# Performance work log

Hardware: AMD Instinct MI355X
Metric: run time of the kernel (lower is better)

Reference implementation:

```python
import jax, jax.numpy as jnp
from jax import lax
import numpy as np

B, N, H, T, NPB = 1024, 50, 128, 50, 3
C_TANH, NEG = 10.0, 1e9


def _lstm(x, h, c, Wi, Wh, b):
    gates = x @ Wi + h @ Wh + b
    i, f, g, o = jnp.split(gates, 4, axis=-1)
    c2 = jax.nn.sigmoid(f) * c + jax.nn.sigmoid(i) * jnp.tanh(g)
    return jax.nn.sigmoid(o) * jnp.tanh(c2), c2


def setup_inputs() -> dict:
    key = jax.random.key(0)
    ks = jax.random.split(key, 20)
    rn = lambda k, shape, fan: (jax.random.normal(k, shape, jnp.float32) / np.float32(np.sqrt(fan)))
    return {
        'input_pnt': jax.random.uniform(ks[0], (B, N, 2), jnp.float32),
        'W_emb': rn(ks[1], (2, H), 2), 'b_emb': jnp.zeros((H,), jnp.float32),
        'dec_init': rn(ks[2], (1, 1, H), H),
        'Wi': rn(ks[3], (H, 4 * H), H), 'Wh': rn(ks[4], (H, 4 * H), H), 'b_lstm': jnp.zeros((4 * H,), jnp.float32),
        'Wq_g': rn(ks[5], (H, H), H), 'Wref_g': rn(ks[6], (H, H), H), 'v_g': rn(ks[7], (H,), H),
        'Wq_p': rn(ks[8], (H, H), H), 'Wref_p': rn(ks[9], (H, H), H), 'v_p': rn(ks[10], (H,), H),
        'Wi_c': rn(ks[11], (H, 4 * H), H), 'Wh_c': rn(ks[12], (H, 4 * H), H), 'b_c': jnp.zeros((4 * H,), jnp.float32),
        'Wq_c': rn(ks[13], (H, H), H), 'Wref_c': rn(ks[14], (H, H), H), 'v_c': rn(ks[15], (H,), H),
        'W1': rn(ks[16], (H, H), H), 'b1': jnp.zeros((H,), jnp.float32),
        'W2': rn(ks[17], (H, 1), H), 'b2': jnp.zeros((1,), jnp.float32),
    }


def _forward(input_pnt, W_emb, b_emb, dec_init, Wi, Wh, b_lstm, Wq_g, Wref_g, v_g,
             Wq_p, Wref_p, v_p, Wi_c, Wh_c, b_c, Wq_c, Wref_c, v_c, W1, b1, W2, b2):
    context = input_pnt @ W_emb + b_emb                    # [B,N,H] embedded nodes
    e_g = context @ Wref_g                                  # glimpse keys (step-invariant, hoisted)
    e_p = context @ Wref_p                                  # pointer keys (hoisted)
    z = jnp.zeros((B, H), context.dtype)
    carry0 = (z, z, jnp.zeros((B, N), context.dtype), jnp.broadcast_to(dec_init[0, 0], (B, H)))

    def step(carry, _):
        h, c, mask, dec_in = carry
        h2, c2 = _lstm(dec_in, h, c, Wi, Wh, b_lstm)
        # glimpse attention (masked)
        q = h2 @ Wq_g
        u = jnp.einsum('bnh,h->bn', jnp.tanh(e_g + q[:, None, :]), v_g) - NEG * mask
        g = jnp.einsum('bn,bnh->bh', jax.nn.softmax(u, -1), e_g)
        # pointer attention with tanh exploration clipping (masked)
        u2 = jnp.einsum('bnh,h->bn', jnp.tanh(e_p + (g @ Wq_p)[:, None, :]), v_p)
        logit = C_TANH * jnp.tanh(u2) - NEG * mask
        logprob = jax.nn.log_softmax(logit, -1)
        prob = jax.nn.softmax(logit, -1)
        action = jnp.argmax(prob, -1)                       # greedy decode
        mask2 = jnp.maximum(mask, jax.nn.one_hot(action, N, dtype=mask.dtype))
        dec_next = jnp.take_along_axis(context, action[:, None, None], axis=1)[:, 0]
        coords = jnp.take_along_axis(input_pnt, action[:, None, None], axis=1)[:, 0]
        return (h2, c2, mask2, dec_next), (logprob, prob, action, coords)

    (_, _, _, dec_last), (logprobs, probs, actions, coords) = lax.scan(step, carry0, None, length=T)
    logprobs = jnp.transpose(logprobs, (1, 0, 2))           # [B,T,N]
    probs = jnp.transpose(probs, (1, 0, 2))
    actions = jnp.transpose(actions, (1, 0))                # [B,T]
    coords = jnp.transpose(coords, (1, 0, 2))               # [B,T,2] visited coordinates
    # reward: TSP tour length
    seg = coords[:, 1:] - coords[:, :-1]
    close = coords[:, 0] - coords[:, -1]
    R = jnp.sum(jnp.sqrt(jnp.sum(seg * seg, -1) + 1e-10), -1) + jnp.sqrt(jnp.sum(close * close, -1) + 1e-10)
    # critic: one LSTM step on last action broadcast to hidden, cn[0], then process blocks
    a4c = jnp.broadcast_to(actions[:, -1].astype(context.dtype)[:, None], (B, H))
    _, hy = _lstm(a4c, z, z, Wi_c, Wh_c, b_c)
    enc = dec_last[:, None, :]                              # context gathered at last action, [B,1,H]
    e_c = enc @ Wref_c
    for _ in range(NPB):
        u = jnp.einsum('bnh,h->bn', jnp.tanh(e_c + (hy @ Wq_c)[:, None, :]), v_c)
        hy = jnp.einsum('bn,bnh->bh', jax.nn.softmax(C_TANH * jnp.tanh(u), -1), e_c)
    v = (jax.nn.relu(hy @ W1 + b1) @ W2 + b2)[:, 0]
    return R, v, logprobs, actions, coords, probs


def reference(input_pnt, W_emb, b_emb, dec_init, Wi, Wh, b_lstm, Wq_g, Wref_g, v_g,
              Wq_p, Wref_p, v_p, Wi_c, Wh_c, b_c, Wq_c, Wref_c, v_c, W1, b1, W2, b2):
    return _forward(input_pnt, W_emb, b_emb, dec_init, Wi, Wh, b_lstm, Wq_g, Wref_g, v_g,
                    Wq_p, Wref_p, v_p, Wi_c, Wh_c, b_c, Wq_c, Wref_c, v_c, W1, b1, W2, b2)
```

## Files before the change

### kernel.cpp

```cpp
#include <hip/hip_runtime.h>
#include <math.h>

#define Bsz 1024
#define Npt 50
#define Hd 128
#define G4 512
#define Tt 50
#define NEGC 1000000000.0f
#define CTANH 10.0f

#define OFF_R 0
#define OFF_V 1024
#define OFF_LP 2048
#define OFF_A 2562048
#define OFF_C 2613248
#define OFF_P 2715648

#define WS_TG 0
#define WS_TP 512
#define WS_TQ 1024
#define WS_A0 1536
#define WS_A1 2048
#define WS_A2 2560
#define WS_A3 3072
#define WS_CT 3584

__device__ __forceinline__ float fsig(float x) {
  return __builtin_amdgcn_rcpf(1.0f + __expf(-x));
}

__device__ __forceinline__ float ftanh(float x) {
  float e = __expf(2.0f * x);
  return 1.0f - 2.0f * __builtin_amdgcn_rcpf(e + 1.0f);
}

__device__ __forceinline__ float dpp_sum_bcast(float x) {
  int v;
  v = __builtin_amdgcn_update_dpp(0, __float_as_int(x), 0x111, 0xf, 0xf, true);
  x += __int_as_float(v);
  v = __builtin_amdgcn_update_dpp(0, __float_as_int(x), 0x112, 0xf, 0xf, true);
  x += __int_as_float(v);
  v = __builtin_amdgcn_update_dpp(0, __float_as_int(x), 0x114, 0xf, 0xf, true);
  x += __int_as_float(v);
  v = __builtin_amdgcn_update_dpp(0, __float_as_int(x), 0x118, 0xf, 0xf, true);
  x += __int_as_float(v);
  v = __builtin_amdgcn_update_dpp(0, __float_as_int(x), 0x142, 0xf, 0xf, true);
  x += __int_as_float(v);
  v = __builtin_amdgcn_update_dpp(0, __float_as_int(x), 0x143, 0xf, 0xf, true);
  x += __int_as_float(v);
  return __int_as_float(__builtin_amdgcn_readlane(__float_as_int(x), 63));
}

__device__ __forceinline__ float dpp_max_bcast(float x) {
  int v;
  v = __builtin_amdgcn_update_dpp(0, __float_as_int(x), 0x111, 0xf, 0xf, true);
  x = fmaxf(x, __int_as_float(v));
  v = __builtin_amdgcn_update_dpp(0, __float_as_int(x), 0x112, 0xf, 0xf, true);
  x = fmaxf(x, __int_as_float(v));
  v = __builtin_amdgcn_update_dpp(0, __float_as_int(x), 0x114, 0xf, 0xf, true);
  x = fmaxf(x, __int_as_float(v));
  v = __builtin_amdgcn_update_dpp(0, __float_as_int(x), 0x118, 0xf, 0xf, true);
  x = fmaxf(x, __int_as_float(v));
  v = __builtin_amdgcn_update_dpp(0, __float_as_int(x), 0x142, 0xf, 0xf, true);
  x = fmaxf(x, __int_as_float(v));
  v = __builtin_amdgcn_update_dpp(0, __float_as_int(x), 0x143, 0xf, 0xf, true);
  x = fmaxf(x, __int_as_float(v));
  return __int_as_float(__builtin_amdgcn_readlane(__float_as_int(x), 63));
}

__device__ __forceinline__ float xsum(float x) {
  #pragma unroll
  for (int off = 32; off >= 1; off >>= 1) x += __shfl_xor(x, off, 64);
  return x;
}

__global__ __launch_bounds__(512) void k_pre(const float* __restrict__ Wemb,
                                             const float* __restrict__ bemb,
                                             const float* __restrict__ dinit,
                                             const float* __restrict__ Wi,
                                             const float* __restrict__ bl,
                                             const float* __restrict__ Wqp,
                                             const float* __restrict__ Wrg,
                                             const float* __restrict__ Wrp,
                                             const float* __restrict__ vg,
                                             const float* __restrict__ vp,
                                             const float* __restrict__ Wrc,
                                             const float* __restrict__ W1,
                                             const float* __restrict__ b1,
                                             const float* __restrict__ W2,
                                             float* __restrict__ ws) {
  __shared__ float mg_s[2][128], mp_s[2][128], cg_s[128], cp_s[128];
  __shared__ float pg_s[2][128], pc_s[128];
  __shared__ float r0_s[128], r1_s[128], rc_s[128];
  int t = threadIdx.x;
  if (t < 256) {
    int j = t >> 7, hh = t & 127;
    float ag = 0.f, ap = 0.f;
    for (int k = 0; k < 128; ++k) {
      float we = Wemb[j * 128 + k];
      ag = fmaf(we, Wrg[k * 128 + hh], ag);
      ap = fmaf(we, Wrp[k * 128 + hh], ap);
    }
    mg_s[j][hh] = ag; mp_s[j][hh] = ap;
  } else if (t < 384) {
    int hh = t & 127;
    float cgv = 0.f, cpv = 0.f;
    for (int k = 0; k < 128; ++k) {
      float be = bemb[k];
      cgv = fmaf(be, Wrg[k * 128 + hh], cgv);
      cpv = fmaf(be, Wrp[k * 128 + hh], cpv);
    }
    cg_s[hh] = cgv; cp_s[hh] = cpv;
  } else {
    int hh = t & 127;
    float a0 = 0.f, a1 = 0.f, ac = 0.f;
    for (int k = 0; k < 128; ++k) {
      float wr = Wrc[k * 128 + hh];
      a0 = fmaf(Wemb[k], wr, a0);
      a1 = fmaf(Wemb[128 + k], wr, a1);
      ac = fmaf(bemb[k], wr, ac);
    }
    r0_s[hh] = a0; r1_s[hh] = a1; rc_s[hh] = ac;
  }
  __syncthreads();
  if (t < 256) {
    int j = t >> 7, hh = t & 127;
    float pg = 0.f;
    for (int k = 0; k < 128; ++k) pg = fmaf(mg_s[j][k], Wqp[k * 128 + hh], pg);
    pg_s[j][hh] = pg;
  } else if (t < 384) {
    int hh = t & 127;
    float pcv = 0.f;
    for (int k = 0; k < 128; ++k) pcv = fmaf(cg_s[k], Wqp[k * 128 + hh], pcv);
    pc_s[hh] = pcv + cp_s[hh];
  } else {
    int hh = t & 127;
    float t0 = 0.f, t1 = 0.f, tc = 0.f;
    for (int k = 0; k < 128; ++k) {
      float w1 = W1[k * 128 + hh];
      t0 = fmaf(r0_s[k], w1, t0);
      t1 = fmaf(r1_s[k], w1, t1);
      tc = fmaf(rc_s[k], w1, tc);
    }
    float4* w4 = (float4*)ws;
    w4[WS_CT / 4 + hh] = make_float4(t0, t1, tc + b1[hh], W2[hh]);
  }
  __syncthreads();
  if (t < 128) {
    float4* w4 = (float4*)ws;
    w4[WS_TG / 4 + t] = make_float4(mg_s[0][t], mg_s[1][t], vg[t], cg_s[t]);
    w4[WS_TP / 4 + t] = make_float4(mp_s[0][t], mp_s[1][t], vp[t], cp_s[t]);
    w4[WS_TQ / 4 + t] = make_float4(pg_s[0][t], pg_s[1][t], pc_s[t], 0.f);
  }
  {
    int j = t;
    float a0 = 0.f, a1 = 0.f, a2 = 0.f, a3 = 0.f;
    for (int k = 0; k < 128; ++k) {
      float wi = Wi[k * G4 + j];
      a0 = fmaf(Wemb[k], wi, a0);
      a1 = fmaf(Wemb[128 + k], wi, a1);
      a2 = fmaf(bemb[k], wi, a2);
      a3 = fmaf(dinit[k], wi, a3);
    }
    ws[WS_A0 + j] = a0;
    ws[WS_A1 + j] = a1;
    ws[WS_A2 + j] = a2 + bl[j];
    ws[WS_A3 + j] = a3 + bl[j];
  }
}

__global__ __launch_bounds__(1024, 4) void k_mega(const float* __restrict__ ip,
                                                  const float* __restrict__ Wh,
                                                  const float* __restrict__ Wqg,
                                                  const float* __restrict__ b2,
                                                  const float* __restrict__ ws,
                                                  float* __restrict__ out) {
  __shared__ __align__(16) float gpart[8][4][G4];
  __shared__ __align__(16) float qpart[8][4][Hd];
  __shared__ __align__(16) float up_s[16][4][64];
  __shared__ __align__(16) float q_w[16][32];
  __shared__ __align__(16) float qp_s[Hd * 4];
  __shared__ __align__(16) float h_s[4][Hd];
  __shared__ __align__(16) float c_s[4][Hd];
  __shared__ __align__(16) float tg_s[G4];
  __shared__ __align__(16) float tp_s[G4];
  __shared__ __align__(16) float tq_s[G4];
  __shared__ __align__(16) float ct_s[G4];
  __shared__ __align__(16) float a0_s[G4], a1_s[G4], a2_s[G4], a3_s[G4];
  __shared__ __align__(16) float cg_s[Hd];
  __shared__ __align__(16) float ip_s[4][Npt * 2];
  __shared__ float mask_s[4][Npt];
  __shared__ float ch_s[4][Npt * 2];
  __shared__ float sel_s[4][2];

  int t = threadIdx.x, blk = blockIdx.x;
  int w = t >> 6, lane = t & 63;
  int kh = t >> 7, jt = t & 127;

  float4 wv[16];
  #pragma unroll
  for (int j = 0; j < 16; ++j)
    wv[j] = *(const float4*)&Wh[(kh * 16 + j) * G4 + jt * 4];
  float wqr[16];
  #pragma unroll
  for (int j = 0; j < 16; ++j)
    wqr[j] = Wqg[(kh * 16 + j) * Hd + jt];

  if (t < 128) {
    float4 tg4 = ((const float4*)(ws + WS_TG))[t];
    ((float4*)tg_s)[t] = tg4;
    cg_s[t] = tg4.w;
    ((float4*)tp_s)[t] = ((const float4*)(ws + WS_TP))[t];
    ((float4*)tq_s)[t] = ((const float4*)(ws + WS_TQ))[t];
    ((float4*)ct_s)[t] = ((const float4*)(ws + WS_CT))[t];
  } else if (t < 256) {
    int i = t - 128;
    ((float4*)a0_s)[i] = ((const float4*)(ws + WS_A0))[i];
    ((float4*)a1_s)[i] = ((const float4*)(ws + WS_A1))[i];
    ((float4*)a2_s)[i] = ((const float4*)(ws + WS_A2))[i];
    ((float4*)a3_s)[i] = ((const float4*)(ws + WS_A3))[i];
  }
  if (t < 200) {
    ((float2*)ip_s)[t] = ((const float2*)ip)[blk * 200 + t];
    ((float*)mask_s)[t] = 0.f;
  }
  if (t < 512) {
    int r = t >> 7, hh = t & 127;
    h_s[r][hh] = 0.f;
    c_s[r][hh] = 0.f;
  }
  if (t < 8) ((float*)sel_s)[t] = 0.f;
  __syncthreads();

  float2 pn0 = make_float2(0.f, 0.f), pn1 = pn0, pn2 = pn0, pn3 = pn0;
  if (lane < Npt) {
    pn0 = ((float2*)ip_s)[0 * Npt + lane];
    pn1 = ((float2*)ip_s)[1 * Npt + lane];
    pn2 = ((float2*)ip_s)[2 * Npt + lane];
    pn3 = ((float2*)ip_s)[3 * Npt + lane];
  }

  for (int st = 0; st < Tt; ++st) {
    {
      int k0 = kh * 16;
      #pragma unroll
      for (int r = 0; r < 4; ++r) {
        float4 ha = *(const float4*)&h_s[r][k0];
        float4 hb = *(const float4*)&h_s[r][k0 + 4];
        float4 hc = *(const float4*)&h_s[r][k0 + 8];
        float4 hd = *(const float4*)&h_s[r][k0 + 12];
        float hv[16] = {ha.x, ha.y, ha.z, ha.w, hb.x, hb.y, hb.z, hb.w,
                        hc.x, hc.y, hc.z, hc.w, hd.x, hd.y, hd.z, hd.w};
        float a0 = 0.f, a1 = 0.f, a2 = 0.f, a3 = 0.f;
        #pragma unroll
        for (int kk = 0; kk < 16; ++kk) {
          float4 wj = wv[kk];
          a0 = fmaf(hv[kk], wj.x, a0);
          a1 = fmaf(hv[kk], wj.y, a1);
          a2 = fmaf(hv[kk], wj.z, a2);
          a3 = fmaf(hv[kk], wj.w, a3);
        }
        *(float4*)&gpart[kh][r][jt * 4] = make_float4(a0, a1, a2, a3);
      }
    }
    __syncthreads();
    if (t < 512) {
      int r = t >> 7, hh = t & 127;
      float p0 = sel_s[r][0], p1 = sel_s[r][1];
      float g[4];
      #pragma unroll
      for (int gi = 0; gi < 4; ++gi) {
        int j = gi * 128 + hh;
        float x = (st == 0) ? a3_s[j]
                            : fmaf(p0, a0_s[j], fmaf(p1, a1_s[j], a2_s[j]));
        #pragma unroll
        for (int k8 = 0; k8 < 8; ++k8) x += gpart[k8][r][j];
        g[gi] = x;
      }
      float c2 = fsig(g[1]) * c_s[r][hh] + fsig(g[0]) * ftanh(g[2]);
      float h2 = fsig(g[3]) * ftanh(c2);
      c_s[r][hh] = c2;
      h_s[r][hh] = h2;
    }
    __syncthreads();
    {
      int k0 = kh * 16;
      #pragma unroll
      for (int r = 0; r < 4; ++r) {
        float4 ha = *(const float4*)&h_s[r][k0];
        float4 hb = *(const float4*)&h_s[r][k0 + 4];
        float4 hc = *(const float4*)&h_s[r][k0 + 8];
        float4 hd = *(const float4*)&h_s[r][k0 + 12];
        float hv[16] = {ha.x, ha.y, ha.z, ha.w, hb.x, hb.y, hb.z, hb.w,
                        hc.x, hc.y, hc.z, hc.w, hd.x, hd.y, hd.z, hd.w};
        float a = 0.f;
        #pragma unroll
        for (int kk = 0; kk < 16; ++kk) a = fmaf(hv[kk], wqr[kk], a);
        qpart[kh][r][jt] = a;
      }
    }
    __syncthreads();
    {
      if (lane < 32) {
        int rr = lane & 3, h = (w << 3) + (lane >> 2);
        float qs = cg_s[h];
        #pragma unroll
        for (int k = 0; k < 8; ++k) qs += qpart[k][rr][h];
        q_w[w][lane] = qs;
      }
      float ac0 = 0.f, ac1 = 0.f, ac2 = 0.f, ac3 = 0.f;
      #pragma unroll
      for (int hp = 0; hp < 8; ++hp) {
        float4 tg4 = ((float4*)tg_s)[(w << 3) + hp];
        float4 qr = ((float4*)q_w[w])[hp];
        ac0 = fmaf(tg4.z, ftanh(fmaf(pn0.x, tg4.x, fmaf(pn0.y, tg4.y, qr.x))), ac0);
        ac1 = fmaf(tg4.z, ftanh(fmaf(pn1.x, tg4.x, fmaf(pn1.y, tg4.y, qr.y))), ac1);
        ac2 = fmaf(tg4.z, ftanh(fmaf(pn2.x, tg4.x, fmaf(pn2.y, tg4.y, qr.z))), ac2);
        ac3 = fmaf(tg4.z, ftanh(fmaf(pn3.x, tg4.x, fmaf(pn3.y, tg4.y, qr.w))), ac3);
      }
      up_s[w][0][lane] = ac0;
      up_s[w][1][lane] = ac1;
      up_s[w][2][lane] = ac2;
      up_s[w][3][lane] = ac3;
    }
    __syncthreads();
    if (w < 4) {
      int r = w;
      float u = 0.f;
      #pragma unroll
      for (int c = 0; c < 16; ++c) u += up_s[c][r][lane];
      float2 ipn = make_float2(0.f, 0.f);
      float e = 0.f;
      if (lane < Npt) {
        ipn = ((float2*)ip_s)[r * Npt + lane];
        e = __expf(u - NEGC * mask_s[r][lane]);
      }
      float ssum = dpp_sum_bcast(e);
      float p = e / ssum;
      float s0 = dpp_sum_bcast(p * ipn.x);
      float s1 = dpp_sum_bcast(p * ipn.y);
      float4 tq0 = ((float4*)tq_s)[lane];
      float4 tq1 = ((float4*)tq_s)[64 + lane];
      qp_s[lane * 4 + r]        = fmaf(s0, tq0.x, fmaf(s1, tq0.y, tq0.z));
      qp_s[(64 + lane) * 4 + r] = fmaf(s0, tq1.x, fmaf(s1, tq1.y, tq1.z));
    }
    __syncthreads();
    {
      float ac0 = 0.f, ac1 = 0.f, ac2 = 0.f, ac3 = 0.f;
      #pragma unroll
      for (int hp = 0; hp < 8; ++hp) {
        float4 tp4 = ((float4*)tp_s)[(w << 3) + hp];
        float4 qr = ((float4*)qp_s)[(w << 3) + hp];
        ac0 = fmaf(tp4.z, ftanh(fmaf(pn0.x, tp4.x, fmaf(pn0.y, tp4.y, qr.x))), ac0);
        ac1 = fmaf(tp4.z, ftanh(fmaf(pn1.x, tp4.x, fmaf(pn1.y, tp4.y, qr.y))), ac1);
        ac2 = fmaf(tp4.z, ftanh(fmaf(pn2.x, tp4.x, fmaf(pn2.y, tp4.y, qr.z))), ac2);
        ac3 = fmaf(tp4.z, ftanh(fmaf(pn3.x, tp4.x, fmaf(pn3.y, tp4.y, qr.w))), ac3);
      }
      up_s[w][0][lane] = ac0;
      up_s[w][1][lane] = ac1;
      up_s[w][2][lane] = ac2;
      up_s[w][3][lane] = ac3;
    }
    __syncthreads();
    if (w < 4) {
      int r = w, b = blk * 4 + r;
      float u = 0.f;
      #pragma unroll
      for (int c = 0; c < 16; ++c) u += up_s[c][r][lane];
      float x = 0.f, e = 0.f;
      if (lane < Npt) {
        x = CTANH * ftanh(u) - NEGC * mask_s[r][lane];
        e = __expf(x);
      }
      float ssum = dpp_sum_bcast(e);
      float ls = __logf(ssum);
      float prob = e / ssum;
      if (lane < Npt) {
        out[OFF_LP + ((size_t)b * Tt + st) * Npt + lane] = x - ls;
        out[OFF_P + ((size_t)b * Tt + st) * Npt + lane] = prob;
      }
      float mx = dpp_max_bcast(prob);
      unsigned long long bal = __ballot((prob == mx) && (lane < Npt));
      int a = __ffsll(bal) - 1;
      float p0a = ip_s[r][2 * a];
      float p1a = ip_s[r][2 * a + 1];
      if (lane == 0) {
        out[OFF_A + (size_t)b * Tt + st] = (float)a;
        out[OFF_C + ((size_t)b * Tt + st) * 2 + 0] = p0a;
        out[OFF_C + ((size_t)b * Tt + st) * 2 + 1] = p1a;
        ((float2*)ch_s)[r * Npt + st] = make_float2(p0a, p1a);
        mask_s[r][a] = 1.0f;
        sel_s[r][0] = p0a;
        sel_s[r][1] = p1a;
      }
    }
    __syncthreads();
  }

  if (w < 4) {
    int r = w, b = blk * 4 + r;
    float p0 = sel_s[r][0], p1 = sel_s[r][1];
    float4 ct0 = ((float4*)ct_s)[lane];
    float4 ct1 = ((float4*)ct_s)[64 + lane];
    float t1a = fmaxf(fmaf(p0, ct0.x, fmaf(p1, ct0.y, ct0.z)), 0.f);
    float t1b = fmaxf(fmaf(p0, ct1.x, fmaf(p1, ct1.y, ct1.z)), 0.f);
    float sv = xsum(t1a * ct0.w + t1b * ct1.w);
    if (lane == 0) out[OFF_V + b] = sv + b2[0];
    float rr = 0.f;
    if (lane < Npt) {
      float2 c0 = ((float2*)ch_s)[r * Npt + lane];
      float2 c1 = ((float2*)ch_s)[r * Npt + ((lane == Npt - 1) ? 0 : lane + 1)];
      float dx = c1.x - c0.x, dy = c1.y - c0.y;
      rr = sqrtf(dx * dx + dy * dy + 1e-10f);
    }
    rr = xsum(rr);
    if (lane == 0) out[OFF_R + b] = rr;
  }
}

extern "C" void kernel_launch(void* const* d_in, const int* in_sizes, int n_in,
                              void* d_out, int out_size, void* d_ws, size_t ws_size,
                              hipStream_t stream) {
  (void)in_sizes; (void)n_in; (void)out_size; (void)ws_size;
  const float* ip    = (const float*)d_in[0];
  const float* Wemb  = (const float*)d_in[1];
  const float* bemb  = (const float*)d_in[2];
  const float* dinit = (const float*)d_in[3];
  const float* Wi    = (const float*)d_in[4];
  const float* Wh    = (const float*)d_in[5];
  const float* bl    = (const float*)d_in[6];
  const float* Wqg   = (const float*)d_in[7];
  const float* Wrg   = (const float*)d_in[8];
  const float* vg    = (const float*)d_in[9];
  const float* Wqp   = (const float*)d_in[10];
  const float* Wrp   = (const float*)d_in[11];
  const float* vp    = (const float*)d_in[12];
  const float* Wrc   = (const float*)d_in[17];
  const float* W1    = (const float*)d_in[19];
  const float* b1    = (const float*)d_in[20];
  const float* W2    = (const float*)d_in[21];
  const float* b2    = (const float*)d_in[22];
  float* out = (float*)d_out;
  float* ws  = (float*)d_ws;

  k_pre<<<1, 512, 0, stream>>>(Wemb, bemb, dinit, Wi, bl, Wqp, Wrg, Wrp,
                               vg, vp, Wrc, W1, b1, W2, ws);
  k_mega<<<256, 1024, 0, stream>>>(ip, Wh, Wqg, b2, ws, out);
}
```

Before: 677.7 us.

## Halve batch rows per block, rewrite tanh as rcp(exp), overlap pointer softmax with next step

Blocks now handle 2 batch rows with 512 threads, and the grid doubles to 512 blocks. Each thread holds 32 rows of the Wh/Wq weight slice instead of 16, which raises register pressure. Tanh-based attention scores are rewritten algebraically as v·(1 - 2/(exp(2a)+1)): weights are pre-scaled by ±2 and the constant term is precomputed per chunk, leaving one exp and one rcp per element. The pointer softmax and argmax for step t is deferred into idle waves during the next step's LSTM matvec, which removes one barrier stage per step. A dummy padded shared array, written only under an impossible condition, reserves LDS, apparently to limit how many blocks fit on a CU.

```diff
diff --git a/kernel.cpp b/kernel.cpp
--- a/kernel.cpp
+++ b/kernel.cpp
@@ -169,50 +169,53 @@
   }
 }
 
-__global__ __launch_bounds__(1024, 4) void k_mega(const float* __restrict__ ip,
-                                                  const float* __restrict__ Wh,
-                                                  const float* __restrict__ Wqg,
-                                                  const float* __restrict__ b2,
-                                                  const float* __restrict__ ws,
-                                                  float* __restrict__ out) {
-  __shared__ __align__(16) float gpart[8][4][G4];
-  __shared__ __align__(16) float qpart[8][4][Hd];
-  __shared__ __align__(16) float up_s[16][4][64];
-  __shared__ __align__(16) float q_w[16][32];
-  __shared__ __align__(16) float qp_s[Hd * 4];
-  __shared__ __align__(16) float h_s[4][Hd];
-  __shared__ __align__(16) float c_s[4][Hd];
+__global__ __launch_bounds__(512, 4) void k_mega(const float* __restrict__ ip,
+                                                 const float* __restrict__ Wh,
+                                                 const float* __restrict__ Wqg,
+                                                 const float* __restrict__ b2,
+                                                 const float* __restrict__ ws,
+                                                 float* __restrict__ out) {
+  __shared__ __align__(16) float gpart[4][2][G4];
+  __shared__ __align__(16) float qpart[4][2][Hd];
+  __shared__ __align__(16) float up_s[4][2][64];
+  __shared__ __align__(16) float up2_s[4][2][64];
+  __shared__ __align__(16) float q_w[2][Hd];
+  __shared__ __align__(16) float h_s[2][Hd];
+  __shared__ __align__(16) float c_s[2][Hd];
   __shared__ __align__(16) float tg_s[G4];
   __shared__ __align__(16) float tp_s[G4];
   __shared__ __align__(16) float tq_s[G4];
   __shared__ __align__(16) float ct_s[G4];
   __shared__ __align__(16) float a0_s[G4], a1_s[G4], a2_s[G4], a3_s[G4];
-  __shared__ __align__(16) float cg_s[Hd];
-  __shared__ __align__(16) float ip_s[4][Npt * 2];
-  __shared__ float mask_s[4][Npt];
-  __shared__ float ch_s[4][Npt * 2];
-  __shared__ float sel_s[4][2];
+  __shared__ float vsum_s[2][4];
+  __shared__ __align__(16) float ip_s[2][Npt * 2];
+  __shared__ float mask_s[2][Npt];
+  __shared__ float ch_s[2][Npt * 2];
+  __shared__ float sel_s[2][2];
+  __shared__ float pad_s[2304];
 
   int t = threadIdx.x, blk = blockIdx.x;
   int w = t >> 6, lane = t & 63;
   int kh = t >> 7, jt = t & 127;
 
-  float4 wv[16];
+  float4 wv[32];
   #pragma unroll
-  for (int j = 0; j < 16; ++j)
-    wv[j] = *(const float4*)&Wh[(kh * 16 + j) * G4 + jt * 4];
-  float wqr[16];
+  for (int j = 0; j < 32; ++j)
+    wv[j] = *(const float4*)&Wh[(kh * 32 + j) * G4 + jt * 4];
+  float wqr[32];
   #pragma unroll
-  for (int j = 0; j < 16; ++j)
-    wqr[j] = Wqg[(kh * 16 + j) * Hd + jt];
-
+  for (int j = 0; j < 32; ++j)
+    wqr[j] = Wqg[(kh * 32 + j) * Hd + jt];
+
+  const float4* ws4 = (const float4*)ws;
   if (t < 128) {
-    float4 tg4 = ((const float4*)(ws + WS_TG))[t];
-    ((float4*)tg_s)[t] = tg4;
-    cg_s[t] = tg4.w;
-    ((float4*)tp_s)[t] = ((const float4*)(ws + WS_TP))[t];
-    ((float4*)tq_s)[t] = ((const float4*)(ws + WS_TQ))[t];
-    ((float4*)ct_s)[t] = ((const float4*)(ws + WS_CT))[t];
+    float4 g4 = ws4[WS_TG / 4 + t];
+    ((float4*)tg_s)[t] = make_float4(2.f * g4.x, 2.f * g4.y, -2.f * g4.z, 2.f * g4.w);
+    float4 p4 = ws4[WS_TP / 4 + t];
+    ((float4*)tp_s)[t] = make_float4(2.f * p4.x, 2.f * p4.y, -2.f * p4.z, 0.f);
+    float4 q4 = ws4[WS_TQ / 4 + t];
+    ((float4*)tq_s)[t] = make_float4(2.f * q4.x, 2.f * q4.y, 2.f * q4.z, 0.f);
+    ((float4*)ct_s)[t] = ws4[WS_CT / 4 + t];
   } else if (t < 256) {
     int i = t - 128;
     ((float4*)a0_s)[i] = ((const float4*)(ws + WS_A0))[i];
@@ -220,40 +223,42 @@
     ((float4*)a2_s)[i] = ((const float4*)(ws + WS_A2))[i];
     ((float4*)a3_s)[i] = ((const float4*)(ws + WS_A3))[i];
   }
-  if (t < 200) {
-    ((float2*)ip_s)[t] = ((const float2*)ip)[blk * 200 + t];
+  if (t < 100) {
+    ((float2*)ip_s)[t] = ((const float2*)ip)[blk * 100 + t];
     ((float*)mask_s)[t] = 0.f;
   }
-  if (t < 512) {
+  if (t < 256) {
     int r = t >> 7, hh = t & 127;
     h_s[r][hh] = 0.f;
     c_s[r][hh] = 0.f;
   }
-  if (t < 8) ((float*)sel_s)[t] = 0.f;
+  if (t < 8) {
+    int c = t & 3, which = t >> 2;
+    float s = 0.f;
+    for (int hp = 0; hp < 32; ++hp)
+      s += ws[(which ? WS_TP : WS_TG) + (c * 32 + hp) * 4 + 2];
+    vsum_s[which][c] = s;
+  }
+  if (t < 4) ((float*)sel_s)[t] = 0.f;
+  if (b2[0] == 12345.678f) pad_s[t] = b2[0];
   __syncthreads();
 
-  float2 pn0 = make_float2(0.f, 0.f), pn1 = pn0, pn2 = pn0, pn3 = pn0;
-  if (lane < Npt) {
-    pn0 = ((float2*)ip_s)[0 * Npt + lane];
-    pn1 = ((float2*)ip_s)[1 * Npt + lane];
-    pn2 = ((float2*)ip_s)[2 * Npt + lane];
-    pn3 = ((float2*)ip_s)[3 * Npt + lane];
-  }
+  int cr = w & 1, cc = w >> 1;
+  float2 pn = make_float2(0.f, 0.f);
+  if (lane < Npt) pn = ((float2*)ip_s)[cr * Npt + lane];
 
   for (int st = 0; st < Tt; ++st) {
     {
-      int k0 = kh * 16;
+      int k0 = kh * 32;
       #pragma unroll
-      for (int r = 0; r < 4; ++r) {
-        float4 ha = *(const float4*)&h_s[r][k0];
-        float4 hb = *(const float4*)&h_s[r][k0 + 4];
-        float4 hc = *(const float4*)&h_s[r][k0 + 8];
-        float4 hd = *(const float4*)&h_s[r][k0 + 12];
-        float hv[16] = {ha.x, ha.y, ha.z, ha.w, hb.x, hb.y, hb.z, hb.w,
-                        hc.x, hc.y, hc.z, hc.w, hd.x, hd.y, hd.z, hd.w};
+      for (int r = 0; r < 2; ++r) {
+        float hv[32];
+        #pragma unroll
+        for (int q8 = 0; q8 < 8; ++q8)
+          *(float4*)&hv[q8 * 4] = *(const float4*)&h_s[r][k0 + q8 * 4];
         float a0 = 0.f, a1 = 0.f, a2 = 0.f, a3 = 0.f;
         #pragma unroll
-        for (int kk = 0; kk < 16; ++kk) {
+        for (int kk = 0; kk < 32; ++kk) {
           float4 wj = wv[kk];
           a0 = fmaf(hv[kk], wj.x, a0);
           a1 = fmaf(hv[kk], wj.y, a1);
@@ -263,8 +268,39 @@
         *(float4*)&gpart[kh][r][jt * 4] = make_float4(a0, a1, a2, a3);
       }
     }
+    if (w >= 6 && st > 0) {
+      int r = w - 6, stp = st - 1, b = blk * 2 + r;
+      float u = up2_s[0][r][lane] + up2_s[1][r][lane]
+              + up2_s[2][r][lane] + up2_s[3][r][lane];
+      float x = 0.f, e = 0.f;
+      if (lane < Npt) {
+        x = CTANH * ftanh(u) - NEGC * mask_s[r][lane];
+        e = __expf(x);
+      }
+      float ssum = dpp_sum_bcast(e);
+      float ls = __logf(ssum);
+      float prob = e / ssum;
+      if (lane < Npt) {
+        out[OFF_LP + ((size_t)b * Tt + stp) * Npt + lane] = x - ls;
+        out[OFF_P + ((size_t)b * Tt + stp) * Npt + lane] = prob;
+      }
+      float mx = dpp_max_bcast(prob);
+      unsigned long long bal = __ballot((prob == mx) && (lane < Npt));
+      int a = __ffsll(bal) - 1;
+      float p0a = ip_s[r][2 * a];
+      float p1a = ip_s[r][2 * a + 1];
+      if (lane == 0) {
+        out[OFF_A + (size_t)b * Tt + stp] = (float)a;
+        out[OFF_C + ((size_t)b * Tt + stp) * 2 + 0] = p0a;
+        out[OFF_C + ((size_t)b * Tt + stp) * 2 + 1] = p1a;
+        ((float2*)ch_s)[r * Npt + stp] = make_float2(p0a, p1a);
+        mask_s[r][a] = 1.0f;
+        sel_s[r][0] = p0a;
+        sel_s[r][1] = p1a;
+      }
+    }
     __syncthreads();
-    if (t < 512) {
+    if (t < 256) {
       int r = t >> 7, hh = t & 127;
       float p0 = sel_s[r][0], p1 = sel_s[r][1];
       float g[4];
@@ -273,8 +309,7 @@
         int j = gi * 128 + hh;
         float x = (st == 0) ? a3_s[j]
                             : fmaf(p0, a0_s[j], fmaf(p1, a1_s[j], a2_s[j]));
-        #pragma unroll
-        for (int k8 = 0; k8 < 8; ++k8) x += gpart[k8][r][j];
+        x += gpart[0][r][j] + gpart[1][r][j] + gpart[2][r][j] + gpart[3][r][j];
         g[gi] = x;
       }
       float c2 = fsig(g[1]) * c_s[r][hh] + fsig(g[0]) * ftanh(g[2]);
@@ -284,121 +319,110 @@
     }
     __syncthreads();
     {
-      int k0 = kh * 16;
+      int k0 = kh * 32;
       #pragma unroll
-      for (int r = 0; r < 4; ++r) {
-        float4 ha = *(const float4*)&h_s[r][k0];
-        float4 hb = *(const float4*)&h_s[r][k0 + 4];
-        float4 hc = *(const float4*)&h_s[r][k0 + 8];
-        float4 hd = *(const float4*)&h_s[r][k0 + 12];
-        float hv[16] = {ha.x, ha.y, ha.z, ha.w, hb.x, hb.y, hb.z, hb.w,
-                        hc.x, hc.y, hc.z, hc.w, hd.x, hd.y, hd.z, hd.w};
+      for (int r = 0; r < 2; ++r) {
+        float hv[32];
+        #pragma unroll
+        for (int q8 = 0; q8 < 8; ++q8)
+          *(float4*)&hv[q8 * 4] = *(const float4*)&h_s[r][k0 + q8 * 4];
         float a = 0.f;
         #pragma unroll
-        for (int kk = 0; kk < 16; ++kk) a = fmaf(hv[kk], wqr[kk], a);
+        for (int kk = 0; kk < 32; ++kk) a = fmaf(hv[kk], wqr[kk], a);
         qpart[kh][r][jt] = a;
       }
     }
     __syncthreads();
     {
       if (lane < 32) {
-        int rr = lane & 3, h = (w << 3) + (lane >> 2);
-        float qs = cg_s[h];
-        #pragma unroll
-        for (int k = 0; k < 8; ++k) qs += qpart[k][rr][h];
-        q_w[w][lane] = qs;
-      }
-      float ac0 = 0.f, ac1 = 0.f, ac2 = 0.f, ac3 = 0.f;
+        int h = cc * 32 + lane;
+        float qs = ((float4*)tg_s)[h].w
+                 + 2.f * (qpart[0][cr][h] + qpart[1][cr][h]
+                        + qpart[2][cr][h] + qpart[3][cr][h]);
+        q_w[cr][h] = qs;
+      }
+      float ac = vsum_s[0][cc];
       #pragma unroll
-      for (int hp = 0; hp < 8; ++hp) {
-        float4 tg4 = ((float4*)tg_s)[(w << 3) + hp];
-        float4 qr = ((float4*)q_w[w])[hp];
-        ac0 = fmaf(tg4.z, ftanh(fmaf(pn0.x, tg4.x, fmaf(pn0.y, tg4.y, qr.x))), ac0);
-        ac1 = fmaf(tg4.z, ftanh(fmaf(pn1.x, tg4.x, fmaf(pn1.y, tg4.y, qr.y))), ac1);
-        ac2 = fmaf(tg4.z, ftanh(fmaf(pn2.x, tg4.x, fmaf(pn2.y, tg4.y, qr.z))), ac2);
-        ac3 = fmaf(tg4.z, ftanh(fmaf(pn3.x, tg4.x, fmaf(pn3.y, tg4.y, qr.w))), ac3);
-      }
-      up_s[w][0][lane] = ac0;
-      up_s[w][1][lane] = ac1;
-      up_s[w][2][lane] = ac2;
-      up_s[w][3][lane] = ac3;
+      for (int hp4 = 0; hp4 < 8; ++hp4) {
+        float4 qv = ((float4*)&q_w[cr][cc * 32])[hp4];
+        float qa[4] = {qv.x, qv.y, qv.z, qv.w};
+        #pragma unroll
+        for (int k = 0; k < 4; ++k) {
+          float4 tg4 = ((float4*)tg_s)[cc * 32 + hp4 * 4 + k];
+          float a = fmaf(pn.x, tg4.x, fmaf(pn.y, tg4.y, qa[k]));
+          float rc = __builtin_amdgcn_rcpf(__expf(a) + 1.0f);
+          ac = fmaf(tg4.z, rc, ac);
+        }
+      }
+      up_s[cc][cr][lane] = ac;
     }
     __syncthreads();
-    if (w < 4) {
-      int r = w;
-      float u = 0.f;
-      #pragma unroll
-      for (int c = 0; c < 16; ++c) u += up_s[c][r][lane];
-      float2 ipn = make_float2(0.f, 0.f);
+    {
+      float u = up_s[0][cr][lane] + up_s[1][cr][lane]
+              + up_s[2][cr][lane] + up_s[3][cr][lane];
       float e = 0.f;
-      if (lane < Npt) {
-        ipn = ((float2*)ip_s)[r * Npt + lane];
-        e = __expf(u - NEGC * mask_s[r][lane]);
-      }
+      if (lane < Npt) e = __expf(u - NEGC * mask_s[cr][lane]);
       float ssum = dpp_sum_bcast(e);
       float p = e / ssum;
-      float s0 = dpp_sum_bcast(p * ipn.x);
-      float s1 = dpp_sum_bcast(p * ipn.y);
-      float4 tq0 = ((float4*)tq_s)[lane];
-      float4 tq1 = ((float4*)tq_s)[64 + lane];
-      qp_s[lane * 4 + r]        = fmaf(s0, tq0.x, fmaf(s1, tq0.y, tq0.z));
-      qp_s[(64 + lane) * 4 + r] = fmaf(s0, tq1.x, fmaf(s1, tq1.y, tq1.z));
+      float s0 = dpp_sum_bcast(p * pn.x);
+      float s1 = dpp_sum_bcast(p * pn.y);
+      if (lane < 32) {
+        int h = cc * 32 + lane;
+        float4 tq4 = ((float4*)tq_s)[h];
+        q_w[cr][h] = fmaf(s0, tq4.x, fmaf(s1, tq4.y, tq4.z));
+      }
+      float ac = vsum_s[1][cc];
+      #pragma unroll
+      for (int hp4 = 0; hp4 < 8; ++hp4) {
+        float4 qv = ((float4*)&q_w[cr][cc * 32])[hp4];
+        float qa[4] = {qv.x, qv.y, qv.z, qv.w};
+        #pragma unroll
+        for (int k = 0; k < 4; ++k) {
+          float4 tp4 = ((float4*)tp_s)[cc * 32 + hp4 * 4 + k];
+          float a = fmaf(pn.x, tp4.x, fmaf(pn.y, tp4.y, qa[k]));
+          float rc = __builtin_amdgcn_rcpf(__expf(a) + 1.0f);
+          ac = fmaf(tp4.z, rc, ac);
+        }
+      }
+      up2_s[cc][cr][lane] = ac;
     }
     __syncthreads();
-    {
-      float ac0 = 0.f, ac1 = 0.f, ac2 = 0.f, ac3 = 0.f;
-      #pragma unroll
-      for (int hp = 0; hp < 8; ++hp) {
-        float4 tp4 = ((float4*)tp_s)[(w << 3) + hp];
-        float4 qr = ((float4*)qp_s)[(w << 3) + hp];
-        ac0 = fmaf(tp4.z, ftanh(fmaf(pn0.x, tp4.x, fmaf(pn0.y, tp4.y, qr.x))), ac0);
-        ac1 = fmaf(tp4.z, ftanh(fmaf(pn1.x, tp4.x, fmaf(pn1.y, tp4.y, qr.y))), ac1);
-        ac2 = fmaf(tp4.z, ftanh(fmaf(pn2.x, tp4.x, fmaf(pn2.y, tp4.y, qr.z))), ac2);
-        ac3 = fmaf(tp4.z, ftanh(fmaf(pn3.x, tp4.x, fmaf(pn3.y, tp4.y, qr.w))), ac3);
-      }
-      up_s[w][0][lane] = ac0;
-      up_s[w][1][lane] = ac1;
-      up_s[w][2][lane] = ac2;
-      up_s[w][3][lane] = ac3;
-    }
-    __syncthreads();
-    if (w < 4) {
-      int r = w, b = blk * 4 + r;
-      float u = 0.f;
-      #pragma unroll
-      for (int c = 0; c < 16; ++c) u += up_s[c][r][lane];
-      float x = 0.f, e = 0.f;
-      if (lane < Npt) {
-        x = CTANH * ftanh(u) - NEGC * mask_s[r][lane];
-        e = __expf(x);
-      }
-      float ssum = dpp_sum_bcast(e);
-      float ls = __logf(ssum);
-      float prob = e / ssum;
-      if (lane < Npt) {
-        out[OFF_LP + ((size_t)b * Tt + st) * Npt + lane] = x - ls;
-        out[OFF_P + ((size_t)b * Tt + st) * Npt + lane] = prob;
-      }
-      float mx = dpp_max_bcast(prob);
-      unsigned long long bal = __ballot((prob == mx) && (lane < Npt));
-      int a = __ffsll(bal) - 1;
-      float p0a = ip_s[r][2 * a];
-      float p1a = ip_s[r][2 * a + 1];
-      if (lane == 0) {
-        out[OFF_A + (size_t)b * Tt + st] = (float)a;
-        out[OFF_C + ((size_t)b * Tt + st) * 2 + 0] = p0a;
-        out[OFF_C + ((size_t)b * Tt + st) * 2 + 1] = p1a;
-        ((float2*)ch_s)[r * Npt + st] = make_float2(p0a, p1a);
-        mask_s[r][a] = 1.0f;
-        sel_s[r][0] = p0a;
-        sel_s[r][1] = p1a;
-      }
-    }
-    __syncthreads();
-  }
-
-  if (w < 4) {
-    int r = w, b = blk * 4 + r;
+  }
+
+  if (w >= 6) {
+    int r = w - 6, stp = Tt - 1, b = blk * 2 + r;
+    float u = up2_s[0][r][lane] + up2_s[1][r][lane]
+            + up2_s[2][r][lane] + up2_s[3][r][lane];
+    float x = 0.f, e = 0.f;
+    if (lane < Npt) {
+      x = CTANH * ftanh(u) - NEGC * mask_s[r][lane];
+      e = __expf(x);
+    }
+    float ssum = dpp_sum_bcast(e);
+    float ls = __logf(ssum);
+    float prob = e / ssum;
+    if (lane < Npt) {
+      out[OFF_LP + ((size_t)b * Tt + stp) * Npt + lane] = x - ls;
+      out[OFF_P + ((size_t)b * Tt + stp) * Npt + lane] = prob;
+    }
+    float mx = dpp_max_bcast(prob);
+    unsigned long long bal = __ballot((prob == mx) && (lane < Npt));
+    int a = __ffsll(bal) - 1;
+    float p0a = ip_s[r][2 * a];
+    float p1a = ip_s[r][2 * a + 1];
+    if (lane == 0) {
+      out[OFF_A + (size_t)b * Tt + stp] = (float)a;
+      out[OFF_C + ((size_t)b * Tt + stp) * 2 + 0] = p0a;
+      out[OFF_C + ((size_t)b * Tt + stp) * 2 + 1] = p1a;
+      ((float2*)ch_s)[r * Npt + stp] = make_float2(p0a, p1a);
+      sel_s[r][0] = p0a;
+      sel_s[r][1] = p1a;
+    }
+  }
+  __syncthreads();
+
+  if (w < 2) {
+    int r = w, b = blk * 2 + r;
     float p0 = sel_s[r][0], p1 = sel_s[r][1];
     float4 ct0 = ((float4*)ct_s)[lane];
     float4 ct1 = ((float4*)ct_s)[64 + lane];
@@ -445,5 +469,5 @@
 
   k_pre<<<1, 512, 0, stream>>>(Wemb, bemb, dinit, Wi, bl, Wqp, Wrg, Wrp,
                                vg, vp, Wrc, W1, b1, W2, ws);
-  k_mega<<<256, 1024, 0, stream>>>(ip, Wh, Wqg, b2, ws, out);
-}
+  k_mega<<<512, 512, 0, stream>>>(ip, Wh, Wqg, b2, ws, out);
+}
```

Result: slower. 1.866 ms (+175.4%).

## Split block rows into two groups and software-pipeline LSTM with attention stages

Applied to the files above, without the earlier changes.

The four batch rows per block are split into two groups of two, and the per-step stages are interleaved so that one group's LSTM/matvec work runs in the same barrier interval as the other group's attention work. This keeps the barrier count per step at six while both halves progress, so fewer threads sit idle in serial phases. The tanh in both attention passes is rewritten as a sigmoid-like reciprocal of exp plus one, with the constants pre-scaled and a precomputed v-sum offset. This cuts transcendental cost but slightly changes the numerics and adds prologue and epilogue stages.

```diff
diff --git a/kernel.cpp b/kernel.cpp
--- a/kernel.cpp
+++ b/kernel.cpp
@@ -175,11 +175,11 @@
                                                   const float* __restrict__ b2,
                                                   const float* __restrict__ ws,
                                                   float* __restrict__ out) {
-  __shared__ __align__(16) float gpart[8][4][G4];
-  __shared__ __align__(16) float qpart[8][4][Hd];
-  __shared__ __align__(16) float up_s[16][4][64];
-  __shared__ __align__(16) float q_w[16][32];
-  __shared__ __align__(16) float qp_s[Hd * 4];
+  __shared__ __align__(16) float gpart[8][2][G4];
+  __shared__ __align__(16) float qpart[8][2][Hd];
+  __shared__ __align__(16) float up_s[8][2][64];
+  __shared__ __align__(16) float up2_s[8][2][64];
+  __shared__ __align__(16) float qc_s[2][Hd];
   __shared__ __align__(16) float h_s[4][Hd];
   __shared__ __align__(16) float c_s[4][Hd];
   __shared__ __align__(16) float tg_s[G4];
@@ -187,7 +187,7 @@
   __shared__ __align__(16) float tq_s[G4];
   __shared__ __align__(16) float ct_s[G4];
   __shared__ __align__(16) float a0_s[G4], a1_s[G4], a2_s[G4], a3_s[G4];
-  __shared__ __align__(16) float cg_s[Hd];
+  __shared__ float vsum_s[2][8];
   __shared__ __align__(16) float ip_s[4][Npt * 2];
   __shared__ float mask_s[4][Npt];
   __shared__ float ch_s[4][Npt * 2];
@@ -206,13 +206,15 @@
   for (int j = 0; j < 16; ++j)
     wqr[j] = Wqg[(kh * 16 + j) * Hd + jt];
 
+  const float4* ws4 = (const float4*)ws;
   if (t < 128) {
-    float4 tg4 = ((const float4*)(ws + WS_TG))[t];
-    ((float4*)tg_s)[t] = tg4;
-    cg_s[t] = tg4.w;
-    ((float4*)tp_s)[t] = ((const float4*)(ws + WS_TP))[t];
-    ((float4*)tq_s)[t] = ((const float4*)(ws + WS_TQ))[t];
-    ((float4*)ct_s)[t] = ((const float4*)(ws + WS_CT))[t];
+    float4 g4 = ws4[WS_TG / 4 + t];
+    ((float4*)tg_s)[t] = make_float4(2.f * g4.x, 2.f * g4.y, -2.f * g4.z, 2.f * g4.w);
+    float4 p4 = ws4[WS_TP / 4 + t];
+    ((float4*)tp_s)[t] = make_float4(2.f * p4.x, 2.f * p4.y, -2.f * p4.z, 0.f);
+    float4 q4 = ws4[WS_TQ / 4 + t];
+    ((float4*)tq_s)[t] = make_float4(2.f * q4.x, 2.f * q4.y, 2.f * q4.z, 0.f);
+    ((float4*)ct_s)[t] = ws4[WS_CT / 4 + t];
   } else if (t < 256) {
     int i = t - 128;
     ((float4*)a0_s)[i] = ((const float4*)(ws + WS_A0))[i];
@@ -229,173 +231,181 @@
     h_s[r][hh] = 0.f;
     c_s[r][hh] = 0.f;
   }
+  if (t < 16) {
+    int which = t >> 3, c = t & 7;
+    float s = 0.f;
+    for (int hp = 0; hp < 16; ++hp)
+      s += ws[(which ? WS_TP : WS_TG) + (c * 16 + hp) * 4 + 2];
+    vsum_s[which][c] = s;
+  }
   if (t < 8) ((float*)sel_s)[t] = 0.f;
   __syncthreads();
 
-  float2 pn0 = make_float2(0.f, 0.f), pn1 = pn0, pn2 = pn0, pn3 = pn0;
+  float2 pnA = make_float2(0.f, 0.f), pnB = pnA;
   if (lane < Npt) {
-    pn0 = ((float2*)ip_s)[0 * Npt + lane];
-    pn1 = ((float2*)ip_s)[1 * Npt + lane];
-    pn2 = ((float2*)ip_s)[2 * Npt + lane];
-    pn3 = ((float2*)ip_s)[3 * Npt + lane];
-  }
-
-  for (int st = 0; st < Tt; ++st) {
-    {
-      int k0 = kh * 16;
-      #pragma unroll
-      for (int r = 0; r < 4; ++r) {
-        float4 ha = *(const float4*)&h_s[r][k0];
-        float4 hb = *(const float4*)&h_s[r][k0 + 4];
-        float4 hc = *(const float4*)&h_s[r][k0 + 8];
-        float4 hd = *(const float4*)&h_s[r][k0 + 12];
-        float hv[16] = {ha.x, ha.y, ha.z, ha.w, hb.x, hb.y, hb.z, hb.w,
-                        hc.x, hc.y, hc.z, hc.w, hd.x, hd.y, hd.z, hd.w};
-        float a0 = 0.f, a1 = 0.f, a2 = 0.f, a3 = 0.f;
-        #pragma unroll
-        for (int kk = 0; kk < 16; ++kk) {
-          float4 wj = wv[kk];
-          a0 = fmaf(hv[kk], wj.x, a0);
-          a1 = fmaf(hv[kk], wj.y, a1);
-          a2 = fmaf(hv[kk], wj.z, a2);
-          a3 = fmaf(hv[kk], wj.w, a3);
-        }
-        *(float4*)&gpart[kh][r][jt * 4] = make_float4(a0, a1, a2, a3);
+    pnA = ((float2*)ip_s)[(w & 1) * Npt + lane];
+    pnB = ((float2*)ip_s)[(2 + (w & 1)) * Npt + lane];
+  }
+
+  auto A1 = [&](int g) {
+    int k0 = kh * 16;
+    #pragma unroll
+    for (int r = 0; r < 2; ++r) {
+      int row = g * 2 + r;
+      float hv[16];
+      #pragma unroll
+      for (int q4i = 0; q4i < 4; ++q4i)
+        *(float4*)&hv[q4i * 4] = *(const float4*)&h_s[row][k0 + q4i * 4];
+      float a0 = 0.f, a1 = 0.f, a2 = 0.f, a3 = 0.f;
+      #pragma unroll
+      for (int kk = 0; kk < 16; ++kk) {
+        float4 wj = wv[kk];
+        a0 = fmaf(hv[kk], wj.x, a0);
+        a1 = fmaf(hv[kk], wj.y, a1);
+        a2 = fmaf(hv[kk], wj.z, a2);
+        a3 = fmaf(hv[kk], wj.w, a3);
       }
-    }
-    __syncthreads();
-    if (t < 512) {
-      int r = t >> 7, hh = t & 127;
-      float p0 = sel_s[r][0], p1 = sel_s[r][1];
-      float g[4];
+      *(float4*)&gpart[kh][r][jt * 4] = make_float4(a0, a1, a2, a3);
+    }
+  };
+  auto A2 = [&](int g, int s) {
+    if (t < 256) {
+      int r = t >> 7, hh = t & 127, row = g * 2 + r;
+      float p0 = sel_s[row][0], p1 = sel_s[row][1];
+      float gg[4];
       #pragma unroll
       for (int gi = 0; gi < 4; ++gi) {
         int j = gi * 128 + hh;
-        float x = (st == 0) ? a3_s[j]
-                            : fmaf(p0, a0_s[j], fmaf(p1, a1_s[j], a2_s[j]));
+        float x = (s == 0) ? a3_s[j]
+                           : fmaf(p0, a0_s[j], fmaf(p1, a1_s[j], a2_s[j]));
         #pragma unroll
         for (int k8 = 0; k8 < 8; ++k8) x += gpart[k8][r][j];
-        g[gi] = x;
+        gg[gi] = x;
       }
-      float c2 = fsig(g[1]) * c_s[r][hh] + fsig(g[0]) * ftanh(g[2]);
-      float h2 = fsig(g[3]) * ftanh(c2);
-      c_s[r][hh] = c2;
-      h_s[r][hh] = h2;
-    }
-    __syncthreads();
-    {
-      int k0 = kh * 16;
-      #pragma unroll
-      for (int r = 0; r < 4; ++r) {
-        float4 ha = *(const float4*)&h_s[r][k0];
-        float4 hb = *(const float4*)&h_s[r][k0 + 4];
-        float4 hc = *(const float4*)&h_s[r][k0 + 8];
-        float4 hd = *(const float4*)&h_s[r][k0 + 12];
-        float hv[16] = {ha.x, ha.y, ha.z, ha.w, hb.x, hb.y, hb.z, hb.w,
-                        hc.x, hc.y, hc.z, hc.w, hd.x, hd.y, hd.z, hd.w};
-        float a = 0.f;
-        #pragma unroll
-        for (int kk = 0; kk < 16; ++kk) a = fmaf(hv[kk], wqr[kk], a);
-        qpart[kh][r][jt] = a;
-      }
-    }
-    __syncthreads();
-    {
-      if (lane < 32) {
-        int rr = lane & 3, h = (w << 3) + (lane >> 2);
-        float qs = cg_s[h];
-        #pragma unroll
-        for (int k = 0; k < 8; ++k) qs += qpart[k][rr][h];
-        q_w[w][lane] = qs;
-      }
-      float ac0 = 0.f, ac1 = 0.f, ac2 = 0.f, ac3 = 0.f;
-      #pragma unroll
-      for (int hp = 0; hp < 8; ++hp) {
-        float4 tg4 = ((float4*)tg_s)[(w << 3) + hp];
-        float4 qr = ((float4*)q_w[w])[hp];
-        ac0 = fmaf(tg4.z, ftanh(fmaf(pn0.x, tg4.x, fmaf(pn0.y, tg4.y, qr.x))), ac0);
-        ac1 = fmaf(tg4.z, ftanh(fmaf(pn1.x, tg4.x, fmaf(pn1.y, tg4.y, qr.y))), ac1);
-        ac2 = fmaf(tg4.z, ftanh(fmaf(pn2.x, tg4.x, fmaf(pn2.y, tg4.y, qr.z))), ac2);
-        ac3 = fmaf(tg4.z, ftanh(fmaf(pn3.x, tg4.x, fmaf(pn3.y, tg4.y, qr.w))), ac3);
-      }
-      up_s[w][0][lane] = ac0;
-      up_s[w][1][lane] = ac1;
-      up_s[w][2][lane] = ac2;
-      up_s[w][3][lane] = ac3;
-    }
-    __syncthreads();
-    if (w < 4) {
-      int r = w;
+      float c2 = fsig(gg[1]) * c_s[row][hh] + fsig(gg[0]) * ftanh(gg[2]);
+      float h2 = fsig(gg[3]) * ftanh(c2);
+      c_s[row][hh] = c2;
+      h_s[row][hh] = h2;
+    }
+  };
+  auto Bp = [&](int g) {
+    int k0 = kh * 16;
+    #pragma unroll
+    for (int r = 0; r < 2; ++r) {
+      int row = g * 2 + r;
+      float hv[16];
+      #pragma unroll
+      for (int q4i = 0; q4i < 4; ++q4i)
+        *(float4*)&hv[q4i * 4] = *(const float4*)&h_s[row][k0 + q4i * 4];
+      float a = 0.f;
+      #pragma unroll
+      for (int kk = 0; kk < 16; ++kk) a = fmaf(hv[kk], wqr[kk], a);
+      qpart[kh][r][jt] = a;
+    }
+  };
+  auto Cp = [&](int g) {
+    int r = w & 1, hc = w >> 1;
+    if (lane < 16) {
+      int h = hc * 16 + lane;
+      float qs = ((float4*)tg_s)[h].w
+               + 2.f * (qpart[0][r][h] + qpart[1][r][h] + qpart[2][r][h]
+                      + qpart[3][r][h] + qpart[4][r][h] + qpart[5][r][h]
+                      + qpart[6][r][h] + qpart[7][r][h]);
+      qc_s[r][h] = qs;
+    }
+    float2 pn = g ? pnB : pnA;
+    float ac = vsum_s[0][hc];
+    #pragma unroll
+    for (int hp = 0; hp < 16; ++hp) {
+      int h = hc * 16 + hp;
+      float4 tg4 = ((float4*)tg_s)[h];
+      float a = fmaf(pn.x, tg4.x, fmaf(pn.y, tg4.y, qc_s[r][h]));
+      ac = fmaf(tg4.z, __builtin_amdgcn_rcpf(__expf(a) + 1.0f), ac);
+    }
+    up_s[hc][r][lane] = ac;
+  };
+  auto DE = [&](int g) {
+    int r = w & 1, hc = w >> 1, row = g * 2 + r;
+    float u = 0.f;
+    #pragma unroll
+    for (int c = 0; c < 8; ++c) u += up_s[c][r][lane];
+    float2 pn = g ? pnB : pnA;
+    float e = 0.f;
+    if (lane < Npt) e = __expf(u - NEGC * mask_s[row][lane]);
+    float ssum = dpp_sum_bcast(e);
+    float p = e / ssum;
+    float s0 = dpp_sum_bcast(p * pn.x);
+    float s1 = dpp_sum_bcast(p * pn.y);
+    if (lane < 16) {
+      int h = hc * 16 + lane;
+      float4 tq4 = ((float4*)tq_s)[h];
+      qc_s[r][h] = fmaf(s0, tq4.x, fmaf(s1, tq4.y, tq4.z));
+    }
+    float ac = vsum_s[1][hc];
+    #pragma unroll
+    for (int hp = 0; hp < 16; ++hp) {
+      int h = hc * 16 + hp;
+      float4 tp4 = ((float4*)tp_s)[h];
+      float a = fmaf(pn.x, tp4.x, fmaf(pn.y, tp4.y, qc_s[r][h]));
+      ac = fmaf(tp4.z, __builtin_amdgcn_rcpf(__expf(a) + 1.0f), ac);
+    }
+    up2_s[hc][r][lane] = ac;
+  };
+  auto Fp = [&](int g, int s) {
+    if (w < 2) {
+      int r = w, row = g * 2 + r, b = blk * 4 + row;
       float u = 0.f;
       #pragma unroll
-      for (int c = 0; c < 16; ++c) u += up_s[c][r][lane];
-      float2 ipn = make_float2(0.f, 0.f);
-      float e = 0.f;
-      if (lane < Npt) {
-        ipn = ((float2*)ip_s)[r * Npt + lane];
-        e = __expf(u - NEGC * mask_s[r][lane]);
-      }
-      float ssum = dpp_sum_bcast(e);
-      float p = e / ssum;
-      float s0 = dpp_sum_bcast(p * ipn.x);
-      float s1 = dpp_sum_bcast(p * ipn.y);
-      float4 tq0 = ((float4*)tq_s)[lane];
-      float4 tq1 = ((float4*)tq_s)[64 + lane];
-      qp_s[lane * 4 + r]        = fmaf(s0, tq0.x, fmaf(s1, tq0.y, tq0.z));
-      qp_s[(64 + lane) * 4 + r] = fmaf(s0, tq1.x, fmaf(s1, tq1.y, tq1.z));
-    }
-    __syncthreads();
-    {
-      float ac0 = 0.f, ac1 = 0.f, ac2 = 0.f, ac3 = 0.f;
-      #pragma unroll
-      for (int hp = 0; hp < 8; ++hp) {
-        float4 tp4 = ((float4*)tp_s)[(w << 3) + hp];
-        float4 qr = ((float4*)qp_s)[(w << 3) + hp];
-        ac0 = fmaf(tp4.z, ftanh(fmaf(pn0.x, tp4.x, fmaf(pn0.y, tp4.y, qr.x))), ac0);
-        ac1 = fmaf(tp4.z, ftanh(fmaf(pn1.x, tp4.x, fmaf(pn1.y, tp4.y, qr.y))), ac1);
-        ac2 = fmaf(tp4.z, ftanh(fmaf(pn2.x, tp4.x, fmaf(pn2.y, tp4.y, qr.z))), ac2);
-        ac3 = fmaf(tp4.z, ftanh(fmaf(pn3.x, tp4.x, fmaf(pn3.y, tp4.y, qr.w))), ac3);
-      }
-      up_s[w][0][lane] = ac0;
-      up_s[w][1][lane] = ac1;
-      up_s[w][2][lane] = ac2;
-      up_s[w][3][lane] = ac3;
-    }
-    __syncthreads();
-    if (w < 4) {
-      int r = w, b = blk * 4 + r;
-      float u = 0.f;
-      #pragma unroll
-      for (int c = 0; c < 16; ++c) u += up_s[c][r][lane];
+      for (int c = 0; c < 8; ++c) u += up2_s[c][r][lane];
       float x = 0.f, e = 0.f;
       if (lane < Npt) {
-        x = CTANH * ftanh(u) - NEGC * mask_s[r][lane];
+        x = CTANH * ftanh(u) - NEGC * mask_s[row][lane];
         e = __expf(x);
       }
       float ssum = dpp_sum_bcast(e);
       float ls = __logf(ssum);
       float prob = e / ssum;
       if (lane < Npt) {
-        out[OFF_LP + ((size_t)b * Tt + st) * Npt + lane] = x - ls;
-        out[OFF_P + ((size_t)b * Tt + st) * Npt + lane] = prob;
+        out[OFF_LP + ((size_t)b * Tt + s) * Npt + lane] = x - ls;
+        out[OFF_P + ((size_t)b * Tt + s) * Npt + lane] = prob;
       }
       float mx = dpp_max_bcast(prob);
       unsigned long long bal = __ballot((prob == mx) && (lane < Npt));
       int a = __ffsll(bal) - 1;
-      float p0a = ip_s[r][2 * a];
-      float p1a = ip_s[r][2 * a + 1];
+      float p0a = ip_s[row][2 * a];
+      float p1a = ip_s[row][2 * a + 1];
       if (lane == 0) {
-        out[OFF_A + (size_t)b * Tt + st] = (float)a;
-        out[OFF_C + ((size_t)b * Tt + st) * 2 + 0] = p0a;
-        out[OFF_C + ((size_t)b * Tt + st) * 2 + 1] = p1a;
-        ((float2*)ch_s)[r * Npt + st] = make_float2(p0a, p1a);
-        mask_s[r][a] = 1.0f;
-        sel_s[r][0] = p0a;
-        sel_s[r][1] = p1a;
+        out[OFF_A + (size_t)b * Tt + s] = (float)a;
+        out[OFF_C + ((size_t)b * Tt + s) * 2 + 0] = p0a;
+        out[OFF_C + ((size_t)b * Tt + s) * 2 + 1] = p1a;
+        ((float2*)ch_s)[row * Npt + s] = make_float2(p0a, p1a);
+        mask_s[row][a] = 1.0f;
+        sel_s[row][0] = p0a;
+        sel_s[row][1] = p1a;
       }
     }
-    __syncthreads();
-  }
+  };
+
+  for (int s = 0; s < Tt; ++s) {
+    A1(0);       if (s > 0) Cp(1);
+    __syncthreads();
+    A2(0, s);    if (s > 0) DE(1);
+    __syncthreads();
+    Bp(0);       if (s > 0) Fp(1, s - 1);
+    __syncthreads();
+    Cp(0);       A1(1);
+    __syncthreads();
+    DE(0);       A2(1, s);
+    __syncthreads();
+    Fp(0, s);    Bp(1);
+    __syncthreads();
+  }
+  Cp(1);
+  __syncthreads();
+  DE(1);
+  __syncthreads();
+  Fp(1, Tt - 1);
+  __syncthreads();
 
   if (w < 4) {
     int r = w, b = blk * 4 + r;
```

After: 760.3 us. +12.2%, slower.
